# Optimization experiments

Hardware: AMD Instinct MI355X
Metric: run time of the kernel (lower is better)

## Reference

```python
import jax, jax.numpy as jnp
import numpy as np

N_P = 50000   # number of 'place' nodes
N_A = 50000   # number of 'a_transition' nodes
E = 1600000   # edges per edge type
IN = 128      # input feature dim
OUT = 64      # HANConv out_channels
H = 4         # heads
D = OUT // H  # per-head dim
HID = 64      # decoder hidden
NEG_SLOPE = 0.2  # HANConv leaky_relu slope


def setup_inputs() -> dict:
    key = jax.random.key(0)
    ks = jax.random.split(key, 24)
    def nrm(i, shape, scale=1.0):
        return jax.random.normal(ks[i], shape, dtype=jnp.float32) * scale
    w = lambda i, shape, fan: nrm(i, shape, (1.0 / fan) ** 0.5)
    return {
        "x_place": nrm(0, (N_P, IN)),
        "x_atrans": nrm(1, (N_A, IN)),
        "e_pa_src": jax.random.randint(ks[2], (E,), 0, N_P),
        "e_pa_dst": jax.random.randint(ks[3], (E,), 0, N_A),
        "e_aa_src": jax.random.randint(ks[4], (E,), 0, N_A),
        "e_aa_dst": jax.random.randint(ks[5], (E,), 0, N_A),
        "e_ap_src": jax.random.randint(ks[6], (E,), 0, N_A),
        "e_ap_dst": jax.random.randint(ks[7], (E,), 0, N_P),
        "Wp_place": w(8, (IN, OUT), IN),
        "bp_place": jnp.zeros((OUT,), jnp.float32),
        "Wp_atrans": w(9, (IN, OUT), IN),
        "bp_atrans": jnp.zeros((OUT,), jnp.float32),
        "asrc_pa": w(10, (H, D), D),
        "adst_pa": w(11, (H, D), D),
        "asrc_aa": w(12, (H, D), D),
        "adst_aa": w(13, (H, D), D),
        "asrc_ap": w(14, (H, D), D),
        "adst_ap": w(15, (H, D), D),
        "Wk": w(16, (OUT, OUT), OUT),
        "bk": jnp.zeros((OUT,), jnp.float32),
        "q": w(17, (OUT,), OUT),
        "Wd1": w(18, (OUT, HID), OUT),
        "bd1": jnp.zeros((HID,), jnp.float32),
        "Wd2": w(19, (HID, 1), HID),
        "bd2": jnp.zeros((1,), jnp.float32),
    }


def _edge_conv(h_src, h_dst, a_src, a_dst, src, dst, n_dst):
    """HANConv node-level attention for one edge type.
    h_src: [N_src, H, D], h_dst: [N_dst, H, D]; returns relu-aggregated [n_dst, H*D]."""
    alpha = (h_src * a_src).sum(-1)[src] + (h_dst * a_dst).sum(-1)[dst]  # [E, H]
    alpha = jax.nn.leaky_relu(alpha, NEG_SLOPE)
    amax = jax.ops.segment_max(alpha, dst, num_segments=n_dst)
    amax = jnp.where(jnp.isfinite(amax), amax, 0.0)  # guard empty neighborhoods
    ex = jnp.exp(alpha - amax[dst])
    den = jax.ops.segment_sum(ex, dst, num_segments=n_dst) + 1e-16  # PyG softmax eps
    wgt = ex / den[dst]                           # scatter-softmax per dst node [E, H]
    msg = h_src[src] * wgt[:, :, None]            # [E, H, D]
    out = jax.ops.segment_sum(msg, dst, num_segments=n_dst)
    return jax.nn.relu(out.reshape(n_dst, H * D))


def _semantic(outs, q, Wk, bk):
    """HANConv semantic-level attention over edge-type embeddings."""
    stk = jnp.stack(outs)                                       # [T, N, OUT]
    score = (q * jnp.tanh(stk @ Wk + bk).mean(axis=1)).sum(-1)  # [T]
    attn = jax.nn.softmax(score)
    return jnp.einsum('t,tnc->nc', attn, stk)


def reference(x_place, x_atrans, e_pa_src, e_pa_dst, e_aa_src, e_aa_dst, e_ap_src, e_ap_dst,
              Wp_place, bp_place, Wp_atrans, bp_atrans,
              asrc_pa, adst_pa, asrc_aa, adst_aa, asrc_ap, adst_ap,
              Wk, bk, q, Wd1, bd1, Wd2, bd2):
    # per-node-type projection, split into heads
    h_p = (x_place @ Wp_place + bp_place).reshape(N_P, H, D)
    h_a = (x_atrans @ Wp_atrans + bp_atrans).reshape(N_A, H, D)
    # node-level attention per edge type
    out_pa = _edge_conv(h_p, h_a, asrc_pa, adst_pa, e_pa_src, e_pa_dst, N_A)
    out_aa = _edge_conv(h_a, h_a, asrc_aa, adst_aa, e_aa_src, e_aa_dst, N_A)
    out_ap = _edge_conv(h_a, h_p, asrc_ap, adst_ap, e_ap_src, e_ap_dst, N_P)
    # semantic-level attention per destination node type
    x_a = _semantic([out_pa, out_aa], q, Wk, bk)   # 'a_transition'
    _xp = _semantic([out_ap], q, Wk, bk)           # 'place' (computed by encoder, unused downstream)
    # decoder MLP on 'a_transition' + softmax over nodes (dim=0)
    z = jax.nn.relu(x_a @ Wd1 + bd1) @ Wd2 + bd2   # [N_A, 1]
    return jax.nn.softmax(z, axis=0)
```

## Files before the change

### kernel.cpp

```cpp
#include <hip/hip_runtime.h>
#include <hip/hip_fp16.h>
#include <math.h>

#define NP 50000
#define NA 50000
#define NE 1600000
#define IN_DIM 128
#define OUT_DIM 64

#define NB 391
#define BCAP 4608
#define P1_CHUNK 4096
#define P1_GRID ((NE + P1_CHUNK - 1) / P1_CHUNK)

typedef _Float16 v8h __attribute__((ext_vector_type(8)));
typedef _Float16 h2f __attribute__((ext_vector_type(2)));
typedef float    v4f __attribute__((ext_vector_type(4)));

__device__ inline float fast_tanh(float x) {
    const float e = __expf(2.f * x);
    return 1.f - 2.f / (e + 1.f);
}

__global__ __launch_bounds__(256) void proj_kernel(
    const float* __restrict__ xA, const float* __restrict__ WA, const float* __restrict__ bA,
    const float* __restrict__ xB, const float* __restrict__ WB, const float* __restrict__ bB,
    const float* __restrict__ a_pa_src, const float* __restrict__ a_pa_dst,
    const float* __restrict__ a_aa_src, const float* __restrict__ a_aa_dst,
    ushort* __restrict__ hA, ushort* __restrict__ hB,
    float* __restrict__ s_p_src_pa, float* __restrict__ s_a_dst_pa,
    float* __restrict__ s_a_src_aa, float* __restrict__ s_a_dst_aa,
    int* __restrict__ gcur, float* __restrict__ sem, float* __restrict__ esum)
{
    const int type = blockIdx.y;
    const float* x = type ? xB : xA;
    const float* W = type ? WB : WA;
    const float* bias = type ? bB : bA;
    ushort* h_out  = type ? hB : hA;
    const float* c0 = type ? a_pa_dst : a_pa_src;
    float*       s0 = type ? s_a_dst_pa : s_p_src_pa;
    const float* c1 = type ? a_aa_src : nullptr;
    float*       s1 = type ? s_a_src_aa : nullptr;
    const float* c2 = type ? a_aa_dst : nullptr;
    float*       s2 = type ? s_a_dst_aa : nullptr;

    if (blockIdx.x == 0 && type == 0) {
        for (int i = threadIdx.x; i < 2 * NB; i += 256) gcur[i] = i * BCAP;
        if (threadIdx.x < 128) sem[threadIdx.x] = 0.f;
        if (threadIdx.x == 0) esum[0] = 0.f;
    }

    __shared__ _Float16 Wt[64][136];
    const int tid = threadIdx.x;
    {
        const float4* W4 = (const float4*)W;
        #pragma unroll
        for (int i = 0; i < 8; ++i) {
            const int f4i = tid + 256 * i;
            const float4 w = W4[f4i];
            const int k = f4i >> 4, c4 = (f4i & 15) * 4;
            Wt[c4 + 0][k] = (_Float16)w.x;
            Wt[c4 + 1][k] = (_Float16)w.y;
            Wt[c4 + 2][k] = (_Float16)w.z;
            Wt[c4 + 3][k] = (_Float16)w.w;
        }
    }
    __syncthreads();

    const int lane = tid & 63;
    const int wid = tid >> 6;
    const int node0 = (blockIdx.x * 4 + wid) * 16;
    if (node0 >= NP) return;
    const int m = lane & 15;
    const int quad = lane >> 4;

    v4f acc[4] = {};
    #pragma unroll
    for (int kc = 0; kc < 4; ++kc) {
        const int k0 = kc * 32 + quad * 8;
        const float4 xa = *(const float4*)(x + (size_t)(node0 + m) * IN_DIM + k0);
        const float4 xb2 = *(const float4*)(x + (size_t)(node0 + m) * IN_DIM + k0 + 4);
        v8h af;
        af[0] = (_Float16)xa.x;  af[1] = (_Float16)xa.y;
        af[2] = (_Float16)xa.z;  af[3] = (_Float16)xa.w;
        af[4] = (_Float16)xb2.x; af[5] = (_Float16)xb2.y;
        af[6] = (_Float16)xb2.z; af[7] = (_Float16)xb2.w;
        #pragma unroll
        for (int cb = 0; cb < 4; ++cb) {
            const v8h bf = *(const v8h*)&Wt[cb * 16 + m][k0];
            acc[cb] = __builtin_amdgcn_mfma_f32_16x16x32_f16(af, bf, acc[cb], 0, 0, 0);
        }
    }

    #pragma unroll
    for (int cb = 0; cb < 4; ++cb) {
        const int c = cb * 16 + m;
        const float bv = bias[c];
        float hv[4];
        #pragma unroll
        for (int r = 0; r < 4; ++r) {
            hv[r] = acc[cb][r] + bv;
            const int node = node0 + quad * 4 + r;
            h_out[(size_t)node * 64 + c] = __half_as_ushort(__float2half_rn(hv[r]));
        }
        #define DO_SCORE(A, S)                                         \
            if (A) {                                                   \
                const float av = (A)[c];                               \
                float v0 = hv[0]*av, v1 = hv[1]*av, v2 = hv[2]*av, v3 = hv[3]*av; \
                for (int msk = 1; msk <= 8; msk <<= 1) {               \
                    v0 += __shfl_xor(v0, msk);                         \
                    v1 += __shfl_xor(v1, msk);                         \
                    v2 += __shfl_xor(v2, msk);                         \
                    v3 += __shfl_xor(v3, msk);                         \
                }                                                      \
                if (m == 0) {                                          \
                    const int nb = node0 + quad * 4;                   \
                    (S)[(nb + 0) * 4 + cb] = v0;                       \
                    (S)[(nb + 1) * 4 + cb] = v1;                       \
                    (S)[(nb + 2) * 4 + cb] = v2;                       \
                    (S)[(nb + 3) * 4 + cb] = v3;                       \
                }                                                      \
            }
        DO_SCORE(c0, s0)
        DO_SCORE(c1, s1)
        DO_SCORE(c2, s2)
        #undef DO_SCORE
    }
}

__global__ __launch_bounds__(256) void partition_kernel(
    const int* __restrict__ srcA, const int* __restrict__ dstA,
    const int* __restrict__ srcB, const int* __restrict__ dstB,
    int* __restrict__ gpart, int* __restrict__ gcur)
{
    const int type = blockIdx.y;
    const int* src = type ? srcB : srcA;
    const int* dst = type ? dstB : dstA;
    const int ebase = blockIdx.x * P1_CHUNK;
    const int ecount = min(P1_CHUNK, NE - ebase);
    const int tid = threadIdx.x;

    __shared__ int hist[NB];
    __shared__ int starts[NB];
    __shared__ int offs2[NB];
    __shared__ int gbase[NB];
    __shared__ int sorted[P1_CHUNK];

    for (int i = tid; i < NB; i += 256) hist[i] = 0;
    __syncthreads();
    for (int i = tid; i < ecount; i += 256)
        atomicAdd(&hist[dst[ebase + i] >> 7], 1);
    __syncthreads();
    if (tid < 64) {
        int carry = 0;
        for (int r = 0; r < 7; ++r) {
            const int idx = r * 64 + tid;
            const int v = (idx < NB) ? hist[idx] : 0;
            int s = v;
            #pragma unroll
            for (int off = 1; off < 64; off <<= 1) {
                const int t = __shfl_up(s, off);
                if (tid >= off) s += t;
            }
            if (idx < NB) { starts[idx] = carry + s - v; offs2[idx] = carry + s - v; }
            carry += __shfl(s, 63);
        }
    }
    __syncthreads();
    for (int i = tid; i < ecount; i += 256) {
        const int d = dst[ebase + i];
        const int s = src[ebase + i];
        const int pos = atomicAdd(&offs2[d >> 7], 1);
        sorted[pos] = ((d & 127) << 16) | s;
    }
    __syncthreads();
    for (int b = tid; b < NB; b += 256) {
        const int cnt = hist[b];
        gbase[b] = cnt ? atomicAdd(&gcur[type * NB + b], cnt) : 0;
    }
    __syncthreads();
    const int wid = tid >> 6, lane = tid & 63;
    for (int b = wid; b < NB; b += 4) {
        const int st = starts[b], cnt = hist[b], gb = gbase[b];
        for (int i = lane; i < cnt; i += 64) gpart[gb + i] = sorted[st + i];
    }
}

__global__ __launch_bounds__(128) void bscan_kernel(
    const int* __restrict__ gcur, int* __restrict__ bstart)
{
    const int w = threadIdx.x >> 6, lane = threadIdx.x & 63;
    int carry = 0;
    for (int r = 0; r < 7; ++r) {
        const int idx = r * 64 + lane;
        const int flat = w * NB + idx;
        const int v = (idx < NB) ? (gcur[flat] - flat * BCAP) : 0;
        int s = v;
        #pragma unroll
        for (int off = 1; off < 64; off <<= 1) {
            const int t = __shfl_up(s, off);
            if (lane >= off) s += t;
        }
        if (idx < NB) bstart[flat] = carry + s - v;
        carry += __shfl(s, 63);
    }
}

__global__ __launch_bounds__(256) void bucket_sort_kernel(
    int* __restrict__ gpart, const int* __restrict__ gcur,
    const int* __restrict__ bstart,
    int* __restrict__ recA, int* __restrict__ offsA,
    int* __restrict__ recB, int* __restrict__ offsB)
{
    const int b = blockIdx.x, type = blockIdx.y;
    int* rec  = type ? recB  : recA;
    int* offs = type ? offsB : offsA;
    const int flat = type * NB + b;
    const int region = flat * BCAP;
    const int cnt = gcur[flat] - region;
    const int bst = bstart[flat];
    const int tid = threadIdx.x;

    __shared__ int hist[128];
    __shared__ int starts[128];
    __shared__ int offs2[128];
    __shared__ int sorted[BCAP];

    if (tid < 128) hist[tid] = 0;
    __syncthreads();
    for (int i = tid; i < cnt; i += 256)
        atomicAdd(&hist[gpart[region + i] >> 16], 1);
    __syncthreads();
    if (tid < 64) {
        int carry = 0;
        for (int r = 0; r < 2; ++r) {
            const int idx = r * 64 + tid;
            const int v = hist[idx];
            int s = v;
            #pragma unroll
            for (int off = 1; off < 64; off <<= 1) {
                const int t = __shfl_up(s, off);
                if (tid >= off) s += t;
            }
            starts[idx] = carry + s - v;
            offs2[idx]  = carry + s - v;
            carry += __shfl(s, 63);
        }
    }
    __syncthreads();
    for (int i = tid; i < cnt; i += 256) {
        const int pk = gpart[region + i];
        const int pos = atomicAdd(&offs2[pk >> 16], 1);
        sorted[pos] = pk & 0xFFFF;
    }
    __syncthreads();
    for (int i = tid; i < cnt; i += 256) rec[bst + i] = sorted[i];
    if (tid < 128) {
        const int n = b * 128 + tid;
        if (n < NA) offs[n] = bst + starts[tid];
    }
    if (b == NB - 1 && tid == 0) offs[NA] = bst + cnt;
}

__global__ __launch_bounds__(256) void gather_kernel(
    const int* __restrict__ offsA, const int* __restrict__ recA,
    const ushort* __restrict__ hA, const float* __restrict__ ssA,
    const float* __restrict__ sdA, float* __restrict__ outA,
    const int* __restrict__ offsB, const int* __restrict__ recB,
    const ushort* __restrict__ hB, const float* __restrict__ ssB,
    const float* __restrict__ sdB, float* __restrict__ outB, int n_dst)
{
    const int type = blockIdx.y;
    const int* offs = type ? offsB : offsA;
    const int* rec  = type ? recB  : recA;
    const ushort* h_src = type ? hB : hA;
    const float* s_src = type ? ssB : ssA;
    const float* s_dst = type ? sdB : sdA;
    float* outbuf = type ? outB : outA;

    const int lane = threadIdx.x & 63;
    const int d = blockIdx.x * 4 + (threadIdx.x >> 6);
    if (d >= n_dst) return;
    const int q = lane & 7;
    const int sub = lane >> 3;
    const int h = q >> 1;
    const float sd = s_dst[d * 4 + h];
    const ushort* hq = h_src + (q << 3);
    const float* ss = s_src + h;
    const int beg = offs[d], end = offs[d + 1];

    float acc[8] = {};
    float wacc = 0.f;
    for (int base = beg; base < end; base += 64) {
        const int c64 = min(64, end - base);
        const int sv = (lane < c64) ? rec[base + lane] : 0;
        const int iters = (c64 + 7) >> 3;
        for (int it = 0; it < iters; ++it) {
            const int idx = it * 8 + sub;
            const int s = __shfl(sv, idx);
            if (idx < c64) {
                float alpha = ss[(size_t)s * 4] + sd;
                alpha = fmaxf(alpha, 0.2f * alpha);
                const float w = __expf(alpha);
                const uint4 pk = *(const uint4*)(hq + ((size_t)s << 6));
                const h2f a0 = __builtin_bit_cast(h2f, pk.x);
                const h2f a1 = __builtin_bit_cast(h2f, pk.y);
                const h2f a2 = __builtin_bit_cast(h2f, pk.z);
                const h2f a3 = __builtin_bit_cast(h2f, pk.w);
                acc[0] = fmaf((float)a0[0], w, acc[0]);
                acc[1] = fmaf((float)a0[1], w, acc[1]);
                acc[2] = fmaf((float)a1[0], w, acc[2]);
                acc[3] = fmaf((float)a1[1], w, acc[3]);
                acc[4] = fmaf((float)a2[0], w, acc[4]);
                acc[5] = fmaf((float)a2[1], w, acc[5]);
                acc[6] = fmaf((float)a3[0], w, acc[6]);
                acc[7] = fmaf((float)a3[1], w, acc[7]);
                wacc += w;
            }
        }
    }
    #pragma unroll
    for (int m = 8; m <= 32; m <<= 1) {
        #pragma unroll
        for (int j = 0; j < 8; ++j) acc[j] += __shfl_xor(acc[j], m);
        wacc += __shfl_xor(wacc, m);
    }
    if (sub == 0) {
        const float inv = 1.f / (wacc + 1e-16f);
        float4 o0, o1;
        o0.x = fmaxf(acc[0] * inv, 0.f);
        o0.y = fmaxf(acc[1] * inv, 0.f);
        o0.z = fmaxf(acc[2] * inv, 0.f);
        o0.w = fmaxf(acc[3] * inv, 0.f);
        o1.x = fmaxf(acc[4] * inv, 0.f);
        o1.y = fmaxf(acc[5] * inv, 0.f);
        o1.z = fmaxf(acc[6] * inv, 0.f);
        o1.w = fmaxf(acc[7] * inv, 0.f);
        float* op = outbuf + (size_t)d * 64 + q * 8;
        *(float4*)op = o0;
        *(float4*)(op + 4) = o1;
    }
}

#define SEM_BLOCKS 512
__global__ __launch_bounds__(256) void semantic_kernel(
    const float* __restrict__ out0, const float* __restrict__ out1,
    const float* __restrict__ Wk, const float* __restrict__ bk,
    float* __restrict__ sem, int n)
{
    __shared__ float Wks[64][64];
    __shared__ float rows[2][4][64];
    const int c = threadIdx.x, ty = threadIdx.y;
    const int tid = ty * 64 + c;
    for (int i = tid; i < 4096; i += 256) ((float*)Wks)[i] = Wk[i];
    const float bkc = bk[c];
    const int ntiles = (n + 3) / 4;
    float acc0 = 0.f, acc1 = 0.f;
    int tile = blockIdx.x;
    float n0 = 0.f, n1 = 0.f;
    {
        const int node = tile * 4 + ty;
        if (node < n) { n0 = out0[(size_t)node * 64 + c]; n1 = out1[(size_t)node * 64 + c]; }
    }
    while (tile < ntiles) {
        __syncthreads();
        rows[0][ty][c] = n0; rows[1][ty][c] = n1;
        __syncthreads();
        const int ntile = tile + gridDim.x;
        if (ntile < ntiles) {
            const int node = ntile * 4 + ty;
            n0 = (node < n) ? out0[(size_t)node * 64 + c] : 0.f;
            n1 = (node < n) ? out1[(size_t)node * 64 + c] : 0.f;
        }
        const int node = tile * 4 + ty;
        if (node < n) {
            float a0 = bkc, a1 = bkc;
            #pragma unroll
            for (int k = 0; k < 64; ++k) {
                const float w = Wks[k][c];
                a0 = fmaf(rows[0][ty][k], w, a0);
                a1 = fmaf(rows[1][ty][k], w, a1);
            }
            acc0 += fast_tanh(a0);
            acc1 += fast_tanh(a1);
        }
        tile = ntile;
    }
    __syncthreads();
    rows[0][ty][c] = acc0; rows[1][ty][c] = acc1;
    __syncthreads();
    if (ty == 0) {
        atomicAdd(&sem[c],      rows[0][0][c] + rows[0][1][c] + rows[0][2][c] + rows[0][3][c]);
        atomicAdd(&sem[64 + c], rows[1][0][c] + rows[1][1][c] + rows[1][2][c] + rows[1][3][c]);
    }
}

__global__ __launch_bounds__(256) void decoder_kernel(
    const float* __restrict__ out0, const float* __restrict__ out1,
    const float* __restrict__ sem, const float* __restrict__ qv,
    const float* __restrict__ Wd1, const float* __restrict__ bd1,
    const float* __restrict__ Wd2, const float* __restrict__ bd2,
    float* __restrict__ z, int n)
{
    __shared__ float xr[4][64];
    __shared__ float attn_s[2];
    const int c = threadIdx.x, ty = threadIdx.y;
    const int node = blockIdx.x * 4 + ty;

    if (ty == 0) {
        float v0 = sem[c] * qv[c];
        float v1 = sem[64 + c] * qv[c];
        for (int off = 32; off >= 1; off >>= 1) {
            v0 += __shfl_xor(v0, off);
            v1 += __shfl_xor(v1, off);
        }
        if (c == 0) {
            const float t0 = v0 / (float)NA, t1 = v1 / (float)NA;
            const float m = fmaxf(t0, t1);
            const float e0 = __expf(t0 - m), e1 = __expf(t1 - m);
            const float inv = 1.f / (e0 + e1);
            attn_s[0] = e0 * inv;
            attn_s[1] = e1 * inv;
        }
    }
    __syncthreads();
    const float a0 = attn_s[0], a1 = attn_s[1];
    if (node < n)
        xr[ty][c] = a0 * out0[(size_t)node * 64 + c] + a1 * out1[(size_t)node * 64 + c];
    __syncthreads();
    if (node >= n) return;
    float acc = bd1[c];
    #pragma unroll
    for (int k = 0; k < 64; ++k)
        acc = fmaf(xr[ty][k], Wd1[k * 64 + c], acc);
    float hv = fmaxf(acc, 0.f) * Wd2[c];
    for (int off = 32; off >= 1; off >>= 1) hv += __shfl_xor(hv, off);
    if (c == 0) z[node] = hv + bd2[0];
}

__global__ __launch_bounds__(256) void softmax_exp_kernel(
    const float* __restrict__ z, float* __restrict__ e,
    float* __restrict__ esum, int n)
{
    float part = 0.f;
    for (int i = blockIdx.x * 256 + threadIdx.x; i < n; i += gridDim.x * 256) {
        const float v = __expf(z[i]);
        e[i] = v;
        part += v;
    }
    for (int off = 32; off >= 1; off >>= 1) part += __shfl_xor(part, off);
    __shared__ float red[4];
    if ((threadIdx.x & 63) == 0) red[threadIdx.x >> 6] = part;
    __syncthreads();
    if (threadIdx.x == 0)
        atomicAdd(esum, red[0] + red[1] + red[2] + red[3]);
}

__global__ __launch_bounds__(256) void softmax_final_kernel(
    const float* __restrict__ e, const float* __restrict__ esum,
    float* __restrict__ out, int n)
{
    const int i = blockIdx.x * 256 + threadIdx.x;
    if (i < n) out[i] = e[i] / (*esum);
}

extern "C" void kernel_launch(void* const* d_in, const int* in_sizes, int n_in,
                              void* d_out, int out_size, void* d_ws, size_t ws_size,
                              hipStream_t stream)
{
    const float* x_place  = (const float*)d_in[0];
    const float* x_atrans = (const float*)d_in[1];
    const int* e_pa_src = (const int*)d_in[2];
    const int* e_pa_dst = (const int*)d_in[3];
    const int* e_aa_src = (const int*)d_in[4];
    const int* e_aa_dst = (const int*)d_in[5];
    const float* Wp_place  = (const float*)d_in[8];
    const float* bp_place  = (const float*)d_in[9];
    const float* Wp_atrans = (const float*)d_in[10];
    const float* bp_atrans = (const float*)d_in[11];
    const float* asrc_pa = (const float*)d_in[12];
    const float* adst_pa = (const float*)d_in[13];
    const float* asrc_aa = (const float*)d_in[14];
    const float* adst_aa = (const float*)d_in[15];
    const float* Wk  = (const float*)d_in[18];
    const float* bk  = (const float*)d_in[19];
    const float* q   = (const float*)d_in[20];
    const float* Wd1 = (const float*)d_in[21];
    const float* bd1 = (const float*)d_in[22];
    const float* Wd2 = (const float*)d_in[23];
    const float* bd2 = (const float*)d_in[24];
    float* out = (float*)d_out;

    float* ws = (float*)d_ws;
    size_t off = 0;
    auto alloc = [&](size_t n) {
        float* p = ws + off; off += (n + 3) & ~(size_t)3; return p;
    };

    ushort* h_p       = (ushort*)alloc((size_t)NP * 32);
    ushort* h_a       = (ushort*)alloc((size_t)NA * 32);
    float* s_p_src_pa = alloc((size_t)NP * 4);
    float* s_a_dst_pa = alloc((size_t)NA * 4);
    float* s_a_src_aa = alloc((size_t)NA * 4);
    float* s_a_dst_aa = alloc((size_t)NA * 4);
    float* out_pa     = alloc((size_t)NA * 64);
    float* out_aa     = alloc((size_t)NA * 64);
    int*   offs_pa    = (int*)alloc(NA + 1);
    int*   offs_aa    = (int*)alloc(NA + 1);
    int*   rec_pa     = (int*)alloc(NE);
    int*   rec_aa     = (int*)alloc(NE);
    int*   gcur       = (int*)alloc(2 * NB);
    int*   bstart     = (int*)alloc(2 * NB);
    float* sem        = alloc(128);
    float* esum       = alloc(4);
    float* zbuf       = alloc(NA);
    float* ebuf       = alloc(NA);
    int* gpart = (int*)out_pa;
    (void)ws_size; (void)in_sizes; (void)n_in; (void)out_size;

    proj_kernel<<<dim3((NP + 63) / 64, 2), 256, 0, stream>>>(
        x_place, Wp_place, bp_place,
        x_atrans, Wp_atrans, bp_atrans,
        asrc_pa, adst_pa, asrc_aa, adst_aa,
        h_p, h_a,
        s_p_src_pa, s_a_dst_pa, s_a_src_aa, s_a_dst_aa,
        gcur, sem, esum);

    partition_kernel<<<dim3(P1_GRID, 2), 256, 0, stream>>>(
        e_pa_src, e_pa_dst, e_aa_src, e_aa_dst, gpart, gcur);
    bscan_kernel<<<1, 128, 0, stream>>>(gcur, bstart);
    bucket_sort_kernel<<<dim3(NB, 2), 256, 0, stream>>>(
        gpart, gcur, bstart, rec_pa, offs_pa, rec_aa, offs_aa);

    gather_kernel<<<dim3((NA + 3) / 4, 2), 256, 0, stream>>>(
        offs_pa, rec_pa, h_p, s_p_src_pa, s_a_dst_pa, out_pa,
        offs_aa, rec_aa, h_a, s_a_src_aa, s_a_dst_aa, out_aa, NA);

    dim3 b64x4(64, 4);
    semantic_kernel<<<SEM_BLOCKS, b64x4, 0, stream>>>(out_pa, out_aa, Wk, bk, sem, NA);
    decoder_kernel<<<NA / 4, b64x4, 0, stream>>>(
        out_pa, out_aa, sem, q, Wd1, bd1, Wd2, bd2, zbuf, NA);
    softmax_exp_kernel<<<196, 256, 0, stream>>>(zbuf, ebuf, esum, NA);
    softmax_final_kernel<<<(NA + 255) / 256, 256, 0, stream>>>(ebuf, esum, out, NA);
}
```

Baseline: 366.8 us.

## Map one destination node per 8 lanes in gather kernel instead of per wavefront

The gather kernel now assigns 8 threads to each destination node (one per 8-wide feature chunk) and loops serially over that node's edges, so a wavefront covers 8 destinations. This drops the batched record load, the shuffle broadcast and the cross-subgroup xor reduction. With about 32 edges per node on average, the serial loop is longer per thread and lanes may diverge when degrees differ. Each edge now needs its own dependent rec load.

```diff
diff --git a/kernel.cpp b/kernel.cpp
--- a/kernel.cpp
+++ b/kernel.cpp
@@ -278,54 +278,43 @@
     const float* s_dst = type ? sdB : sdA;
     float* outbuf = type ? outB : outA;
 
-    const int lane = threadIdx.x & 63;
-    const int d = blockIdx.x * 4 + (threadIdx.x >> 6);
-    if (d >= n_dst) return;
-    const int q = lane & 7;
-    const int sub = lane >> 3;
+    const int q = threadIdx.x & 7;
+    const int d = blockIdx.x * 32 + (threadIdx.x >> 3);
     const int h = q >> 1;
-    const float sd = s_dst[d * 4 + h];
+    const bool live = d < n_dst;
+    int beg = 0, end = 0;
+    float sd = 0.f;
+    if (live) {
+        beg = offs[d];
+        end = offs[d + 1];
+        sd = s_dst[d * 4 + h];
+    }
     const ushort* hq = h_src + (q << 3);
     const float* ss = s_src + h;
-    const int beg = offs[d], end = offs[d + 1];
 
     float acc[8] = {};
     float wacc = 0.f;
-    for (int base = beg; base < end; base += 64) {
-        const int c64 = min(64, end - base);
-        const int sv = (lane < c64) ? rec[base + lane] : 0;
-        const int iters = (c64 + 7) >> 3;
-        for (int it = 0; it < iters; ++it) {
-            const int idx = it * 8 + sub;
-            const int s = __shfl(sv, idx);
-            if (idx < c64) {
-                float alpha = ss[(size_t)s * 4] + sd;
-                alpha = fmaxf(alpha, 0.2f * alpha);
-                const float w = __expf(alpha);
-                const uint4 pk = *(const uint4*)(hq + ((size_t)s << 6));
-                const h2f a0 = __builtin_bit_cast(h2f, pk.x);
-                const h2f a1 = __builtin_bit_cast(h2f, pk.y);
-                const h2f a2 = __builtin_bit_cast(h2f, pk.z);
-                const h2f a3 = __builtin_bit_cast(h2f, pk.w);
-                acc[0] = fmaf((float)a0[0], w, acc[0]);
-                acc[1] = fmaf((float)a0[1], w, acc[1]);
-                acc[2] = fmaf((float)a1[0], w, acc[2]);
-                acc[3] = fmaf((float)a1[1], w, acc[3]);
-                acc[4] = fmaf((float)a2[0], w, acc[4]);
-                acc[5] = fmaf((float)a2[1], w, acc[5]);
-                acc[6] = fmaf((float)a3[0], w, acc[6]);
-                acc[7] = fmaf((float)a3[1], w, acc[7]);
-                wacc += w;
-            }
-        }
-    }
-    #pragma unroll
-    for (int m = 8; m <= 32; m <<= 1) {
-        #pragma unroll
-        for (int j = 0; j < 8; ++j) acc[j] += __shfl_xor(acc[j], m);
-        wacc += __shfl_xor(wacc, m);
-    }
-    if (sub == 0) {
+    for (int i = beg; i < end; ++i) {
+        const int s = rec[i];
+        float alpha = ss[(size_t)s * 4] + sd;
+        alpha = fmaxf(alpha, 0.2f * alpha);
+        const float w = __expf(alpha);
+        const uint4 pk = *(const uint4*)(hq + ((size_t)s << 6));
+        const h2f a0 = __builtin_bit_cast(h2f, pk.x);
+        const h2f a1 = __builtin_bit_cast(h2f, pk.y);
+        const h2f a2 = __builtin_bit_cast(h2f, pk.z);
+        const h2f a3 = __builtin_bit_cast(h2f, pk.w);
+        acc[0] = fmaf((float)a0[0], w, acc[0]);
+        acc[1] = fmaf((float)a0[1], w, acc[1]);
+        acc[2] = fmaf((float)a1[0], w, acc[2]);
+        acc[3] = fmaf((float)a1[1], w, acc[3]);
+        acc[4] = fmaf((float)a2[0], w, acc[4]);
+        acc[5] = fmaf((float)a2[1], w, acc[5]);
+        acc[6] = fmaf((float)a3[0], w, acc[6]);
+        acc[7] = fmaf((float)a3[1], w, acc[7]);
+        wacc += w;
+    }
+    if (live) {
         const float inv = 1.f / (wacc + 1e-16f);
         float4 o0, o1;
         o0.x = fmaxf(acc[0] * inv, 0.f);
@@ -532,7 +521,7 @@
     bucket_sort_kernel<<<dim3(NB, 2), 256, 0, stream>>>(
         gpart, gcur, bstart, rec_pa, offs_pa, rec_aa, offs_aa);
 
-    gather_kernel<<<dim3((NA + 3) / 4, 2), 256, 0, stream>>>(
+    gather_kernel<<<dim3((NA + 31) / 32, 2), 256, 0, stream>>>(
         offs_pa, rec_pa, h_p, s_p_src_pa, s_a_dst_pa, out_pa,
         offs_aa, rec_aa, h_a, s_a_src_aa, s_a_dst_aa, out_aa, NA);
 
```

New measurement: 387.5 us. 1.06x slower.

## Fuse edge partition and projection into one kernel with memset init

Applied to the files above, without the earlier changes.

Merges the edge-partition pass and the node projection into a single launch, with blocks selected by blockIdx.x, so the two independent workloads run concurrently and one launch is saved. The gcur/sem/esum initialization moves to a hipMemsetAsync, which lets gcur hold counts relative to each bucket region instead of absolute positions. The scan and bucket-sort kernels are adjusted to match. This adds a memset launch, and the shared-memory union is sized for the larger partition footprint, which could reduce occupancy for the projection blocks.

```diff
diff --git a/kernel.cpp b/kernel.cpp
--- a/kernel.cpp
+++ b/kernel.cpp
@@ -12,6 +12,7 @@
 #define BCAP 4608
 #define P1_CHUNK 4096
 #define P1_GRID ((NE + P1_CHUNK - 1) / P1_CHUNK)
+#define PROJ_BLOCKS ((NP + 63) / 64)
 
 typedef _Float16 v8h __attribute__((ext_vector_type(8)));
 typedef _Float16 h2f __attribute__((ext_vector_type(2)));
@@ -22,7 +23,7 @@
     return 1.f - 2.f / (e + 1.f);
 }
 
-__global__ __launch_bounds__(256) void proj_kernel(
+__global__ __launch_bounds__(256) void front_kernel(
     const float* __restrict__ xA, const float* __restrict__ WA, const float* __restrict__ bA,
     const float* __restrict__ xB, const float* __restrict__ WB, const float* __restrict__ bB,
     const float* __restrict__ a_pa_src, const float* __restrict__ a_pa_dst,
@@ -30,9 +31,69 @@
     ushort* __restrict__ hA, ushort* __restrict__ hB,
     float* __restrict__ s_p_src_pa, float* __restrict__ s_a_dst_pa,
     float* __restrict__ s_a_src_aa, float* __restrict__ s_a_dst_aa,
-    int* __restrict__ gcur, float* __restrict__ sem, float* __restrict__ esum)
-{
+    const int* __restrict__ srcA, const int* __restrict__ dstA,
+    const int* __restrict__ srcB, const int* __restrict__ dstB,
+    int* __restrict__ gpart, int* __restrict__ gcur)
+{
+    __shared__ __align__(16) char smem[22656];
     const int type = blockIdx.y;
+    const int tid = threadIdx.x;
+
+    if (blockIdx.x < P1_GRID) {
+        const int* src = type ? srcB : srcA;
+        const int* dst = type ? dstB : dstA;
+        const int ebase = blockIdx.x * P1_CHUNK;
+        const int ecount = min(P1_CHUNK, NE - ebase);
+
+        int* hist   = (int*)smem;
+        int* starts = hist + NB;
+        int* offs2  = starts + NB;
+        int* gbase  = offs2 + NB;
+        int* sorted = gbase + NB;
+
+        for (int i = tid; i < NB; i += 256) hist[i] = 0;
+        __syncthreads();
+        for (int i = tid; i < ecount; i += 256)
+            atomicAdd(&hist[dst[ebase + i] >> 7], 1);
+        __syncthreads();
+        if (tid < 64) {
+            int carry = 0;
+            for (int r = 0; r < 7; ++r) {
+                const int idx = r * 64 + tid;
+                const int v = (idx < NB) ? hist[idx] : 0;
+                int s = v;
+                #pragma unroll
+                for (int off = 1; off < 64; off <<= 1) {
+                    const int t = __shfl_up(s, off);
+                    if (tid >= off) s += t;
+                }
+                if (idx < NB) { starts[idx] = carry + s - v; offs2[idx] = carry + s - v; }
+                carry += __shfl(s, 63);
+            }
+        }
+        __syncthreads();
+        for (int i = tid; i < ecount; i += 256) {
+            const int d = dst[ebase + i];
+            const int s = src[ebase + i];
+            const int pos = atomicAdd(&offs2[d >> 7], 1);
+            sorted[pos] = ((d & 127) << 16) | s;
+        }
+        __syncthreads();
+        for (int b = tid; b < NB; b += 256) {
+            const int cnt = hist[b];
+            const int flatb = type * NB + b;
+            gbase[b] = cnt ? (flatb * BCAP + atomicAdd(&gcur[flatb], cnt)) : 0;
+        }
+        __syncthreads();
+        const int wid = tid >> 6, lane = tid & 63;
+        for (int b = wid; b < NB; b += 4) {
+            const int st = starts[b], cnt = hist[b], gb = gbase[b];
+            for (int i = lane; i < cnt; i += 64) gpart[gb + i] = sorted[st + i];
+        }
+        return;
+    }
+
+    const int pbid = blockIdx.x - P1_GRID;
     const float* x = type ? xB : xA;
     const float* W = type ? WB : WA;
     const float* bias = type ? bB : bA;
@@ -44,14 +105,7 @@
     const float* c2 = type ? a_aa_dst : nullptr;
     float*       s2 = type ? s_a_dst_aa : nullptr;
 
-    if (blockIdx.x == 0 && type == 0) {
-        for (int i = threadIdx.x; i < 2 * NB; i += 256) gcur[i] = i * BCAP;
-        if (threadIdx.x < 128) sem[threadIdx.x] = 0.f;
-        if (threadIdx.x == 0) esum[0] = 0.f;
-    }
-
-    __shared__ _Float16 Wt[64][136];
-    const int tid = threadIdx.x;
+    _Float16 (*Wt)[136] = (_Float16(*)[136])smem;
     {
         const float4* W4 = (const float4*)W;
         #pragma unroll
@@ -69,7 +123,7 @@
 
     const int lane = tid & 63;
     const int wid = tid >> 6;
-    const int node0 = (blockIdx.x * 4 + wid) * 16;
+    const int node0 = (pbid * 4 + wid) * 16;
     if (node0 >= NP) return;
     const int m = lane & 15;
     const int quad = lane >> 4;
@@ -128,64 +182,6 @@
     }
 }
 
-__global__ __launch_bounds__(256) void partition_kernel(
-    const int* __restrict__ srcA, const int* __restrict__ dstA,
-    const int* __restrict__ srcB, const int* __restrict__ dstB,
-    int* __restrict__ gpart, int* __restrict__ gcur)
-{
-    const int type = blockIdx.y;
-    const int* src = type ? srcB : srcA;
-    const int* dst = type ? dstB : dstA;
-    const int ebase = blockIdx.x * P1_CHUNK;
-    const int ecount = min(P1_CHUNK, NE - ebase);
-    const int tid = threadIdx.x;
-
-    __shared__ int hist[NB];
-    __shared__ int starts[NB];
-    __shared__ int offs2[NB];
-    __shared__ int gbase[NB];
-    __shared__ int sorted[P1_CHUNK];
-
-    for (int i = tid; i < NB; i += 256) hist[i] = 0;
-    __syncthreads();
-    for (int i = tid; i < ecount; i += 256)
-        atomicAdd(&hist[dst[ebase + i] >> 7], 1);
-    __syncthreads();
-    if (tid < 64) {
-        int carry = 0;
-        for (int r = 0; r < 7; ++r) {
-            const int idx = r * 64 + tid;
-            const int v = (idx < NB) ? hist[idx] : 0;
-            int s = v;
-            #pragma unroll
-            for (int off = 1; off < 64; off <<= 1) {
-                const int t = __shfl_up(s, off);
-                if (tid >= off) s += t;
-            }
-            if (idx < NB) { starts[idx] = carry + s - v; offs2[idx] = carry + s - v; }
-            carry += __shfl(s, 63);
-        }
-    }
-    __syncthreads();
-    for (int i = tid; i < ecount; i += 256) {
-        const int d = dst[ebase + i];
-        const int s = src[ebase + i];
-        const int pos = atomicAdd(&offs2[d >> 7], 1);
-        sorted[pos] = ((d & 127) << 16) | s;
-    }
-    __syncthreads();
-    for (int b = tid; b < NB; b += 256) {
-        const int cnt = hist[b];
-        gbase[b] = cnt ? atomicAdd(&gcur[type * NB + b], cnt) : 0;
-    }
-    __syncthreads();
-    const int wid = tid >> 6, lane = tid & 63;
-    for (int b = wid; b < NB; b += 4) {
-        const int st = starts[b], cnt = hist[b], gb = gbase[b];
-        for (int i = lane; i < cnt; i += 64) gpart[gb + i] = sorted[st + i];
-    }
-}
-
 __global__ __launch_bounds__(128) void bscan_kernel(
     const int* __restrict__ gcur, int* __restrict__ bstart)
 {
@@ -194,7 +190,7 @@
     for (int r = 0; r < 7; ++r) {
         const int idx = r * 64 + lane;
         const int flat = w * NB + idx;
-        const int v = (idx < NB) ? (gcur[flat] - flat * BCAP) : 0;
+        const int v = (idx < NB) ? gcur[flat] : 0;
         int s = v;
         #pragma unroll
         for (int off = 1; off < 64; off <<= 1) {
@@ -217,7 +213,7 @@
     int* offs = type ? offsB : offsA;
     const int flat = type * NB + b;
     const int region = flat * BCAP;
-    const int cnt = gcur[flat] - region;
+    const int cnt = gcur[flat];
     const int bst = bstart[flat];
     const int tid = threadIdx.x;
 
@@ -510,24 +506,25 @@
     int*   rec_pa     = (int*)alloc(NE);
     int*   rec_aa     = (int*)alloc(NE);
     int*   gcur       = (int*)alloc(2 * NB);
-    int*   bstart     = (int*)alloc(2 * NB);
     float* sem        = alloc(128);
     float* esum       = alloc(4);
+    int*   bstart     = (int*)alloc(2 * NB);
     float* zbuf       = alloc(NA);
     float* ebuf       = alloc(NA);
     int* gpart = (int*)out_pa;
     (void)ws_size; (void)in_sizes; (void)n_in; (void)out_size;
 
-    proj_kernel<<<dim3((NP + 63) / 64, 2), 256, 0, stream>>>(
+    const size_t zbytes = (size_t)((char*)(esum + 4) - (char*)gcur);
+    hipMemsetAsync(gcur, 0, zbytes, stream);
+
+    front_kernel<<<dim3(P1_GRID + PROJ_BLOCKS, 2), 256, 0, stream>>>(
         x_place, Wp_place, bp_place,
         x_atrans, Wp_atrans, bp_atrans,
         asrc_pa, adst_pa, asrc_aa, adst_aa,
         h_p, h_a,
         s_p_src_pa, s_a_dst_pa, s_a_src_aa, s_a_dst_aa,
-        gcur, sem, esum);
-
-    partition_kernel<<<dim3(P1_GRID, 2), 256, 0, stream>>>(
         e_pa_src, e_pa_dst, e_aa_src, e_aa_dst, gpart, gcur);
+
     bscan_kernel<<<1, 128, 0, stream>>>(gcur, bstart);
     bucket_sort_kernel<<<dim3(NB, 2), 256, 0, stream>>>(
         gpart, gcur, bstart, rec_pa, offs_pa, rec_aa, offs_aa);
```

New measurement: 352.5 us. -3.9%, faster.
